# Performance work log

Hardware: AMD Instinct MI355X
Metric: run time of the kernel (lower is better)

The kernel has to match this reference:

```python
import jax, jax.numpy as jnp
import numpy as np

N = 100000
SAMPLE = 25
FEAT = 128
HIDDEN = 128
CLASSES = 40


def setup_inputs() -> dict:
    key = jax.random.key(0)
    k_x, k_n, k_w1, k_w2, k_wl = jax.random.split(key, 5)
    X = jax.random.normal(k_x, (N, FEAT), dtype=jnp.float32)
    neighbors = jax.random.randint(k_n, (N, SAMPLE), 0, N, dtype=jnp.int32)
    # torch Linear weights are [out_features, in_features], xavier-uniform init
    def xavier(k, out_d, in_d):
        bound = float(np.sqrt(6.0 / (in_d + out_d)))
        return jax.random.uniform(k, (out_d, in_d), dtype=jnp.float32, minval=-bound, maxval=bound)
    W1 = xavier(k_w1, HIDDEN, FEAT)
    W2 = xavier(k_w2, HIDDEN, HIDDEN)
    Wlast = xavier(k_wl, CLASSES, HIDDEN)
    return {"X": X, "neighbors": neighbors, "W1": W1, "W2": W2, "Wlast": Wlast}


def reference(X, neighbors, W1, W2, Wlast):
    # forward: for each layer W: X = spmm(adj, X); X = X @ W.T; relu(X)
    # adj row i has sample_num entries of value 1/sample_num -> mean over sampled neighbors
    h = X
    for W in (W1, W2):
        agg = jnp.mean(h[neighbors], axis=1)          # [N, sample, d] -> [N, d]
        h = jax.nn.relu(jnp.einsum('nd,hd->nh', agg, W))
    return jnp.einsum('nh,ch->nc', h, Wlast)          # [N, class_num]
```

## Files before the change

### kernel.cpp

```cpp
#include <hip/hip_runtime.h>
#include <cstdint>
#include <cstddef>

typedef unsigned short u16;
typedef __bf16 bf16x8 __attribute__((ext_vector_type(8)));
typedef u16 u16x8 __attribute__((ext_vector_type(8)));
typedef float f32x4 __attribute__((ext_vector_type(4)));

#define N_NODES 100000
#define SAMPLE 25
#define FEAT 128
#define CLASSES 40

__device__ __forceinline__ float bf2f(u16 v) {
    return __uint_as_float(((unsigned)v) << 16);
}
__device__ __forceinline__ u16 f2bf(float f) {
    unsigned u = __float_as_uint(f);
    u += 0x7FFFu + ((u >> 16) & 1u);
    return (u16)(u >> 16);
}
__device__ __forceinline__ void split_bf(float x, u16& hi, u16& lo) {
    hi = f2bf(x);
    lo = f2bf(x - bf2f(hi));
}

__device__ __forceinline__ void split8(const float* ap, bf16x8& ah, bf16x8& al) {
    union { u16x8 u; bf16x8 b; } H, L;
    #pragma unroll
    for (int j = 0; j < 8; ++j) {
        u16 h, lo; split_bf(ap[j], h, lo);
        H.u[j] = h; L.u[j] = lo;
    }
    ah = H.b; al = L.b;
}

__device__ __forceinline__ f32x4 mfma_split(bf16x8 ah, bf16x8 al,
                                            bf16x8 bh, bf16x8 bl, f32x4 acc) {
    acc = __builtin_amdgcn_mfma_f32_16x16x32_bf16(ah, bh, acc, 0, 0, 0);
    acc = __builtin_amdgcn_mfma_f32_16x16x32_bf16(al, bh, acc, 0, 0, 0);
    acc = __builtin_amdgcn_mfma_f32_16x16x32_bf16(ah, bl, acc, 0, 0, 0);
    return acc;
}

__device__ __forceinline__ void cex(int& a, int& b) {
    int lo = a < b ? a : b;
    int hi = a < b ? b : a;
    a = lo; b = hi;
}

__device__ __forceinline__ void sort32(int* v) {
    #pragma unroll
    for (int p = 1; p < 32; p <<= 1) {
        #pragma unroll
        for (int k = p; k >= 1; k >>= 1) {
            #pragma unroll
            for (int j = k & (p - 1); j + k < 32; j += 2 * k) {
                #pragma unroll
                for (int i = 0; i < k; ++i) {
                    if (j + i + k < 32) {
                        if (((j + i) / (2 * p)) == ((j + i + k) / (2 * p)))
                            cex(v[j + i], v[j + i + k]);
                    }
                }
            }
        }
    }
}

__global__ __launch_bounds__(256) void prep_weights(
    const float* __restrict__ W1, const float* __restrict__ W2,
    const float* __restrict__ Wl,
    u16* __restrict__ w1h, u16* __restrict__ w1l,
    u16* __restrict__ w2h, u16* __restrict__ w2l,
    u16* __restrict__ wlh, u16* __restrict__ wll)
{
    const int i = blockIdx.x * 256 + threadIdx.x;
    const int stride = gridDim.x * 256;
    for (int j = i; j < FEAT * FEAT; j += stride) {
        split_bf(W1[j], w1h[j], w1l[j]);
        split_bf(W2[j], w2h[j], w2l[j]);
    }
    for (int j = i; j < CLASSES * FEAT; j += stride) {
        split_bf(Wl[j], wlh[j], wll[j]);
    }
}

#define NPB32 32
#define ZT_STRIDE 136

__global__ __launch_bounds__(128, 4) void k1_gemm(
    const float* __restrict__ X,
    const u16* __restrict__ w1h, const u16* __restrict__ w1l,
    u16* __restrict__ Z1)
{
    __shared__ u16 zt[NPB32][ZT_STRIDE];

    const int t = threadIdx.x;
    const int w  = t >> 6;
    const int l  = t & 63;
    const int lr = l & 15;
    const int lq = l >> 4;
    const int blockStart = blockIdx.x * NPB32;
    const float* Xrow = X + (size_t)(blockStart + w * 16 + lr) * FEAT;

    bf16x8 ah[4], al[4];
    #pragma unroll
    for (int k = 0; k < 4; ++k) {
        f32x4 x0 = *(const f32x4*)(Xrow + k * 32 + lq * 8);
        f32x4 x1 = *(const f32x4*)(Xrow + k * 32 + lq * 8 + 4);
        float tmp[8];
        #pragma unroll
        for (int j = 0; j < 4; ++j) { tmp[j] = x0[j]; tmp[4 + j] = x1[j]; }
        split8(tmp, ah[k], al[k]);
    }

    #pragma unroll
    for (int c = 0; c < 8; ++c) {
        f32x4 acc = {0.f, 0.f, 0.f, 0.f};
        #pragma unroll
        for (int k = 0; k < 4; ++k) {
            const size_t off = (size_t)(c * 16 + lr) * FEAT + k * 32 + lq * 8;
            bf16x8 bh = *(const bf16x8*)(w1h + off);
            bf16x8 bl = *(const bf16x8*)(w1l + off);
            acc = mfma_split(ah[k], al[k], bh, bl, acc);
        }
        #pragma unroll
        for (int r = 0; r < 4; ++r)
            zt[w * 16 + lq * 4 + r][c * 16 + lr] = f2bf(acc[r]);
    }
    __syncthreads();

    #pragma unroll
    for (int p = 0; p < 4; ++p) {
        const int idx = p * 128 + t;
        const int row = idx >> 4;
        const int col = (idx & 15) * 8;
        *(u16x8*)(Z1 + (size_t)(blockStart + row) * FEAT + col) =
            *(const u16x8*)&zt[row][col];
    }
}

__global__ __launch_bounds__(128, 3) void k2_hop(
    const u16* __restrict__ Zin, const int* __restrict__ nb,
    const u16* __restrict__ wh, const u16* __restrict__ wl,
    u16* __restrict__ Zout)
{
    __shared__ int nbs[NPB32 * SAMPLE];
    __shared__ float agg[NPB32][132];

    const int t = threadIdx.x;
    const int blockStart = blockIdx.x * NPB32;

    for (int i = t; i < NPB32 * SAMPLE; i += 128)
        nbs[i] = nb[blockStart * SAMPLE + i];
    __syncthreads();

    if (t < NPB32) {
        int v[32];
        #pragma unroll
        for (int s = 0; s < SAMPLE; ++s) v[s] = nbs[t * SAMPLE + s];
        #pragma unroll
        for (int s = SAMPLE; s < 32; ++s) v[s] = 0x7FFFFFFF;
        sort32(v);
        #pragma unroll
        for (int s = 0; s < SAMPLE; ++s) nbs[t * SAMPLE + s] = v[s];
    }
    __syncthreads();

    #pragma unroll 1
    for (int it = 0; it < 4; ++it) {
        const int item = t + it * 128;
        const int nl = item >> 4;
        const int fg = item & 15;
        const int* myn = &nbs[nl * SAMPLE];
        u16x8 buf[SAMPLE];
        #pragma unroll
        for (int s = 0; s < SAMPLE; ++s)
            buf[s] = *(const u16x8*)(Zin + ((size_t)myn[s] << 7) + fg * 8);
        float acc[8];
        #pragma unroll
        for (int j = 0; j < 8; ++j) acc[j] = 0.f;
        #pragma unroll
        for (int s = 0; s < SAMPLE; ++s) {
            #pragma unroll
            for (int j = 0; j < 8; ++j) acc[j] += bf2f(buf[s][j]);
        }
        #pragma unroll
        for (int j = 0; j < 8; ++j) {
            float m = acc[j] * (1.0f / SAMPLE);
            agg[nl][fg * 8 + j] = m > 0.f ? m : 0.f;
        }
    }
    __syncthreads();

    const int w  = t >> 6;
    const int l  = t & 63;
    const int lr = l & 15;
    const int lq = l >> 4;

    bf16x8 ah[4], al[4];
    #pragma unroll
    for (int k = 0; k < 4; ++k)
        split8(&agg[w * 16 + lr][k * 32 + lq * 8], ah[k], al[k]);
    __syncthreads();

    u16* zt = (u16*)agg;

    #pragma unroll
    for (int c = 0; c < 8; ++c) {
        f32x4 acc = {0.f, 0.f, 0.f, 0.f};
        #pragma unroll
        for (int k = 0; k < 4; ++k) {
            const size_t off = (size_t)(c * 16 + lr) * FEAT + k * 32 + lq * 8;
            bf16x8 bh = *(const bf16x8*)(wh + off);
            bf16x8 bl = *(const bf16x8*)(wl + off);
            acc = mfma_split(ah[k], al[k], bh, bl, acc);
        }
        #pragma unroll
        for (int r = 0; r < 4; ++r)
            zt[(size_t)(w * 16 + lq * 4 + r) * ZT_STRIDE + c * 16 + lr] = f2bf(acc[r]);
    }
    __syncthreads();

    #pragma unroll
    for (int p = 0; p < 4; ++p) {
        const int idx = p * 128 + t;
        const int row = idx >> 4;
        const int col = (idx & 15) * 8;
        *(u16x8*)(Zout + (size_t)(blockStart + row) * FEAT + col) =
            *(const u16x8*)&zt[(size_t)row * ZT_STRIDE + col];
    }
}

__global__ __launch_bounds__(128, 3) void k3_hop(
    const u16* __restrict__ Zin, const int* __restrict__ nb,
    const u16* __restrict__ wh, const u16* __restrict__ wl,
    float* __restrict__ out)
{
    __shared__ int nbs[NPB32 * SAMPLE];
    __shared__ float agg[NPB32][132];

    const int t = threadIdx.x;
    const int blockStart = blockIdx.x * NPB32;

    for (int i = t; i < NPB32 * SAMPLE; i += 128)
        nbs[i] = nb[blockStart * SAMPLE + i];
    __syncthreads();

    if (t < NPB32) {
        int v[32];
        #pragma unroll
        for (int s = 0; s < SAMPLE; ++s) v[s] = nbs[t * SAMPLE + s];
        #pragma unroll
        for (int s = SAMPLE; s < 32; ++s) v[s] = 0x7FFFFFFF;
        sort32(v);
        #pragma unroll
        for (int s = 0; s < SAMPLE; ++s) nbs[t * SAMPLE + s] = v[s];
    }
    __syncthreads();

    #pragma unroll 1
    for (int it = 0; it < 4; ++it) {
        const int item = t + it * 128;
        const int nl = item >> 4;
        const int fg = item & 15;
        const int* myn = &nbs[nl * SAMPLE];
        u16x8 buf[SAMPLE];
        #pragma unroll
        for (int s = 0; s < SAMPLE; ++s)
            buf[s] = *(const u16x8*)(Zin + ((size_t)myn[s] << 7) + fg * 8);
        float acc[8];
        #pragma unroll
        for (int j = 0; j < 8; ++j) acc[j] = 0.f;
        #pragma unroll
        for (int s = 0; s < SAMPLE; ++s) {
            #pragma unroll
            for (int j = 0; j < 8; ++j) acc[j] += bf2f(buf[s][j]);
        }
        #pragma unroll
        for (int j = 0; j < 8; ++j) {
            float m = acc[j] * (1.0f / SAMPLE);
            agg[nl][fg * 8 + j] = m > 0.f ? m : 0.f;
        }
    }
    __syncthreads();

    const int w  = t >> 6;
    const int l  = t & 63;
    const int lr = l & 15;
    const int lq = l >> 4;

    bf16x8 ah[4], al[4];
    #pragma unroll
    for (int k = 0; k < 4; ++k)
        split8(&agg[w * 16 + lr][k * 32 + lq * 8], ah[k], al[k]);

    #pragma unroll
    for (int c = 0; c < 3; ++c) {
        const int o = c * 16 + lr;
        f32x4 acc = {0.f, 0.f, 0.f, 0.f};
        #pragma unroll
        for (int k = 0; k < 4; ++k) {
            bf16x8 bh, bl;
            if (o < CLASSES) {
                const size_t off = (size_t)o * FEAT + k * 32 + lq * 8;
                bh = *(const bf16x8*)(wh + off);
                bl = *(const bf16x8*)(wl + off);
            } else {
                #pragma unroll
                for (int j = 0; j < 8; ++j) { bh[j] = (__bf16)0.f; bl[j] = (__bf16)0.f; }
            }
            acc = mfma_split(ah[k], al[k], bh, bl, acc);
        }
        if (o < CLASSES) {
            #pragma unroll
            for (int r = 0; r < 4; ++r) {
                const int node = blockStart + w * 16 + lq * 4 + r;
                out[(size_t)node * CLASSES + o] = acc[r];
            }
        }
    }
}

#define NPB 64
#define AGG_STRIDE 136

__global__ __launch_bounds__(256) void gnn_layer1(
    const float* __restrict__ X, const int* __restrict__ nb,
    const u16* __restrict__ w1h, const u16* __restrict__ w1l,
    u16* __restrict__ h1)
{
    __shared__ int nbs[NPB * SAMPLE];
    __shared__ u16 agg_h[NPB][AGG_STRIDE];
    __shared__ u16 agg_l[NPB][AGG_STRIDE];

    const int t = threadIdx.x;
    const int blockStart = blockIdx.x * NPB;

    for (int i = t; i < NPB * SAMPLE; i += 256) {
        int gi = blockStart * SAMPLE + i;
        if (gi >= N_NODES * SAMPLE) gi = N_NODES * SAMPLE - 1;
        nbs[i] = nb[gi];
    }
    __syncthreads();

    for (int item = t; item < NPB * 16; item += 256) {
        const int nl = item >> 4;
        const int fg = item & 15;
        float acc[8];
        #pragma unroll
        for (int j = 0; j < 8; ++j) acc[j] = 0.f;
        const int* myn = &nbs[nl * SAMPLE];
        for (int s = 0; s < SAMPLE; ++s) {
            const float4* p = (const float4*)(X + (size_t)myn[s] * FEAT + fg * 8);
            float4 a = p[0], b = p[1];
            acc[0] += a.x; acc[1] += a.y; acc[2] += a.z; acc[3] += a.w;
            acc[4] += b.x; acc[5] += b.y; acc[6] += b.z; acc[7] += b.w;
        }
        u16x8 oh, ol;
        #pragma unroll
        for (int j = 0; j < 8; ++j) {
            float m = acc[j] * (1.0f / SAMPLE);
            u16 h, lo; split_bf(m, h, lo);
            oh[j] = h; ol[j] = lo;
        }
        *(u16x8*)&agg_h[nl][fg * 8] = oh;
        *(u16x8*)&agg_l[nl][fg * 8] = ol;
    }
    __syncthreads();

    const int w  = t >> 6;
    const int l  = t & 63;
    const int lr = l & 15;
    const int lq = l >> 4;

    bf16x8 ah[4], al[4];
    #pragma unroll
    for (int k = 0; k < 4; ++k) {
        ah[k] = *(const bf16x8*)&agg_h[w * 16 + lr][k * 32 + lq * 8];
        al[k] = *(const bf16x8*)&agg_l[w * 16 + lr][k * 32 + lq * 8];
    }

    #pragma unroll
    for (int c = 0; c < 8; ++c) {
        f32x4 acc = {0.f, 0.f, 0.f, 0.f};
        #pragma unroll
        for (int k = 0; k < 4; ++k) {
            const size_t off = (size_t)(c * 16 + lr) * FEAT + k * 32 + lq * 8;
            bf16x8 bh = *(const bf16x8*)(w1h + off);
            bf16x8 bl = *(const bf16x8*)(w1l + off);
            acc = mfma_split(ah[k], al[k], bh, bl, acc);
        }
        #pragma unroll
        for (int r = 0; r < 4; ++r) {
            int node = blockStart + w * 16 + lq * 4 + r;
            if (node < N_NODES) {
                float v = acc[r] > 0.f ? acc[r] : 0.f;
                h1[(size_t)node * FEAT + c * 16 + lr] = f2bf(v);
            }
        }
    }
}

__global__ __launch_bounds__(256) void gnn_layer2_final(
    const u16* __restrict__ h1, const int* __restrict__ nb,
    const u16* __restrict__ w2h, const u16* __restrict__ w2l,
    const u16* __restrict__ wlh, const u16* __restrict__ wll,
    float* __restrict__ out)
{
    __shared__ int nbs[NPB * SAMPLE];
    __shared__ u16 agg_h[NPB][AGG_STRIDE];
    __shared__ u16 agg_l[NPB][AGG_STRIDE];

    const int t = threadIdx.x;
    const int blockStart = blockIdx.x * NPB;

    for (int i = t; i < NPB * SAMPLE; i += 256) {
        int gi = blockStart * SAMPLE + i;
        if (gi >= N_NODES * SAMPLE) gi = N_NODES * SAMPLE - 1;
        nbs[i] = nb[gi];
    }
    __syncthreads();

    for (int item = t; item < NPB * 16; item += 256) {
        const int nl = item >> 4;
        const int fg = item & 15;
        float acc[8];
        #pragma unroll
        for (int j = 0; j < 8; ++j) acc[j] = 0.f;
        const int* myn = &nbs[nl * SAMPLE];
        for (int s = 0; s < SAMPLE; ++s) {
            u16x8 v = *(const u16x8*)(h1 + (size_t)myn[s] * FEAT + fg * 8);
            #pragma unroll
            for (int j = 0; j < 8; ++j) acc[j] += bf2f(v[j]);
        }
        u16x8 oh, ol;
        #pragma unroll
        for (int j = 0; j < 8; ++j) {
            float m = acc[j] * (1.0f / SAMPLE);
            u16 h, lo; split_bf(m, h, lo);
            oh[j] = h; ol[j] = lo;
        }
        *(u16x8*)&agg_h[nl][fg * 8] = oh;
        *(u16x8*)&agg_l[nl][fg * 8] = ol;
    }
    __syncthreads();

    const int w  = t >> 6;
    const int l  = t & 63;
    const int lr = l & 15;
    const int lq = l >> 4;

    f32x4 hacc[8];
    {
        bf16x8 ah[4], al[4];
        #pragma unroll
        for (int k = 0; k < 4; ++k) {
            ah[k] = *(const bf16x8*)&agg_h[w * 16 + lr][k * 32 + lq * 8];
            al[k] = *(const bf16x8*)&agg_l[w * 16 + lr][k * 32 + lq * 8];
        }
        #pragma unroll
        for (int c = 0; c < 8; ++c) {
            f32x4 acc = {0.f, 0.f, 0.f, 0.f};
            #pragma unroll
            for (int k = 0; k < 4; ++k) {
                const size_t off = (size_t)(c * 16 + lr) * FEAT + k * 32 + lq * 8;
                bf16x8 bh = *(const bf16x8*)(w2h + off);
                bf16x8 bl = *(const bf16x8*)(w2l + off);
                acc = mfma_split(ah[k], al[k], bh, bl, acc);
            }
            hacc[c] = acc;
        }
    }
    __syncthreads();

    #pragma unroll
    for (int c = 0; c < 8; ++c) {
        #pragma unroll
        for (int r = 0; r < 4; ++r) {
            float v = hacc[c][r] > 0.f ? hacc[c][r] : 0.f;
            u16 h, l2; split_bf(v, h, l2);
            agg_h[w * 16 + lq * 4 + r][c * 16 + lr] = h;
            agg_l[w * 16 + lq * 4 + r][c * 16 + lr] = l2;
        }
    }
    __syncthreads();

    {
        bf16x8 ah[4], al[4];
        #pragma unroll
        for (int k = 0; k < 4; ++k) {
            ah[k] = *(const bf16x8*)&agg_h[w * 16 + lr][k * 32 + lq * 8];
            al[k] = *(const bf16x8*)&agg_l[w * 16 + lr][k * 32 + lq * 8];
        }
        #pragma unroll
        for (int c = 0; c < 3; ++c) {
            const int o = c * 16 + lr;
            f32x4 acc = {0.f, 0.f, 0.f, 0.f};
            #pragma unroll
            for (int k = 0; k < 4; ++k) {
                bf16x8 bh, bl;
                if (o < CLASSES) {
                    const size_t off = (size_t)o * FEAT + k * 32 + lq * 8;
                    bh = *(const bf16x8*)(wlh + off);
                    bl = *(const bf16x8*)(wll + off);
                } else {
                    #pragma unroll
                    for (int j = 0; j < 8; ++j) { bh[j] = (__bf16)0.f; bl[j] = (__bf16)0.f; }
                }
                acc = mfma_split(ah[k], al[k], bh, bl, acc);
            }
            if (o < CLASSES) {
                #pragma unroll
                for (int r = 0; r < 4; ++r) {
                    int node = blockStart + w * 16 + lq * 4 + r;
                    if (node < N_NODES) {
                        out[(size_t)node * CLASSES + o] = acc[r];
                    }
                }
            }
        }
    }
}

extern "C" void kernel_launch(void* const* d_in, const int* in_sizes, int n_in,
                              void* d_out, int out_size, void* d_ws, size_t ws_size,
                              hipStream_t stream) {
    const float* X  = (const float*)d_in[0];
    const int*   nb = (const int*)d_in[1];
    const float* W1 = (const float*)d_in[2];
    const float* W2 = (const float*)d_in[3];
    const float* Wl = (const float*)d_in[4];
    float* out = (float*)d_out;

    const size_t zelems = (size_t)N_NODES * FEAT;
    const size_t welems = 4 * (size_t)FEAT * FEAT + 2 * (size_t)CLASSES * FEAT;
    const size_t need_fast = (2 * zelems + welems) * sizeof(u16);

    if (ws_size >= need_fast) {
        u16* Z1  = (u16*)d_ws;
        u16* Z2  = Z1 + zelems;
        u16* w1h = Z2 + zelems;
        u16* w1l = w1h + FEAT * FEAT;
        u16* w2h = w1l + FEAT * FEAT;
        u16* w2l = w2h + FEAT * FEAT;
        u16* wlh = w2l + FEAT * FEAT;
        u16* wll = wlh + CLASSES * FEAT;

        prep_weights<<<64, 256, 0, stream>>>(W1, W2, Wl, w1h, w1l, w2h, w2l, wlh, wll);
        const int blocks = N_NODES / NPB32;
        k1_gemm<<<blocks, 128, 0, stream>>>(X, w1h, w1l, Z1);
        k2_hop<<<blocks, 128, 0, stream>>>(Z1, nb, w2h, w2l, Z2);
        k3_hop<<<blocks, 128, 0, stream>>>(Z2, nb, wlh, wll, out);
    } else {
        u16* h1  = (u16*)d_ws;
        u16* w1h = h1 + zelems;
        u16* w1l = w1h + FEAT * FEAT;
        u16* w2h = w1l + FEAT * FEAT;
        u16* w2l = w2h + FEAT * FEAT;
        u16* wlh = w2l + FEAT * FEAT;
        u16* wll = wlh + CLASSES * FEAT;

        prep_weights<<<64, 256, 0, stream>>>(W1, W2, Wl, w1h, w1l, w2h, w2l, wlh, wll);
        const int blocks = (N_NODES + NPB - 1) / NPB;
        gnn_layer1<<<blocks, 256, 0, stream>>>(X, nb, w1h, w1l, h1);
        gnn_layer2_final<<<blocks, 256, 0, stream>>>(h1, nb, w2h, w2l, wlh, wll, out);
    }
}
```

Measured before the change: 330.1 us.

## Process gather in address-range chunks across two node groups per block

The hop kernels now handle two 32-node groups per block and walk the sorted neighbor lists in 16 row-range chunks. Every block tends to touch the same region of the feature table at the same time, so L2 reuse should improve. The price is a serialized per-item while loop, where the old code issued 25 loads up front; this lowers memory-level parallelism. It also holds 64 float accumulators per thread, which adds register pressure, and the grid is halved.

```diff
diff --git a/kernel.cpp b/kernel.cpp
--- a/kernel.cpp
+++ b/kernel.cpp
@@ -141,95 +141,138 @@
     }
 }
 
+#define GPB 2
+#define NGROUPS 3125
+#define NCHUNK 16
+#define CHUNK 6250
+#define K23_GRID ((NGROUPS + GPB - 1) / GPB)
+
 __global__ __launch_bounds__(128, 3) void k2_hop(
     const u16* __restrict__ Zin, const int* __restrict__ nb,
     const u16* __restrict__ wh, const u16* __restrict__ wl,
     u16* __restrict__ Zout)
 {
-    __shared__ int nbs[NPB32 * SAMPLE];
-    __shared__ float agg[NPB32][132];
+    __shared__ __align__(16) char smem[NPB32 * 130 * 4];
+    int*   nbs = (int*)smem;
+    float (*agg)[130] = (float(*)[130])smem;
 
     const int t = threadIdx.x;
-    const int blockStart = blockIdx.x * NPB32;
-
-    for (int i = t; i < NPB32 * SAMPLE; i += 128)
-        nbs[i] = nb[blockStart * SAMPLE + i];
-    __syncthreads();
-
-    if (t < NPB32) {
+    const int bg0 = blockIdx.x * GPB;
+
+    for (int i = t; i < GPB * NPB32 * SAMPLE; i += 128) {
+        const int g = i / (NPB32 * SAMPLE);
+        const int r = i - g * (NPB32 * SAMPLE);
+        const int gid = bg0 + g;
+        nbs[i] = (gid < NGROUPS) ? nb[(size_t)gid * (NPB32 * SAMPLE) + r] : 0;
+    }
+    __syncthreads();
+
+    if (t < GPB * NPB32) {
+        const int g = t >> 5, nl = t & 31;
         int v[32];
         #pragma unroll
-        for (int s = 0; s < SAMPLE; ++s) v[s] = nbs[t * SAMPLE + s];
+        for (int s = 0; s < SAMPLE; ++s) v[s] = nbs[g * (NPB32 * SAMPLE) + nl * SAMPLE + s];
         #pragma unroll
         for (int s = SAMPLE; s < 32; ++s) v[s] = 0x7FFFFFFF;
         sort32(v);
         #pragma unroll
-        for (int s = 0; s < SAMPLE; ++s) nbs[t * SAMPLE + s] = v[s];
-    }
-    __syncthreads();
+        for (int s = 0; s < SAMPLE; ++s) nbs[g * (NPB32 * SAMPLE) + nl * SAMPLE + s] = v[s];
+    }
+    __syncthreads();
+
+    float acc[GPB][4][8];
+    int   ptr[GPB][4];
+    #pragma unroll
+    for (int g = 0; g < GPB; ++g)
+        #pragma unroll
+        for (int it = 0; it < 4; ++it) {
+            ptr[g][it] = 0;
+            #pragma unroll
+            for (int j = 0; j < 8; ++j) acc[g][it][j] = 0.f;
+        }
 
     #pragma unroll 1
-    for (int it = 0; it < 4; ++it) {
-        const int item = t + it * 128;
-        const int nl = item >> 4;
-        const int fg = item & 15;
-        const int* myn = &nbs[nl * SAMPLE];
-        u16x8 buf[SAMPLE];
-        #pragma unroll
-        for (int s = 0; s < SAMPLE; ++s)
-            buf[s] = *(const u16x8*)(Zin + ((size_t)myn[s] << 7) + fg * 8);
-        float acc[8];
-        #pragma unroll
-        for (int j = 0; j < 8; ++j) acc[j] = 0.f;
-        #pragma unroll
-        for (int s = 0; s < SAMPLE; ++s) {
-            #pragma unroll
-            for (int j = 0; j < 8; ++j) acc[j] += bf2f(buf[s][j]);
-        }
-        #pragma unroll
-        for (int j = 0; j < 8; ++j) {
-            float m = acc[j] * (1.0f / SAMPLE);
-            agg[nl][fg * 8 + j] = m > 0.f ? m : 0.f;
-        }
-    }
-    __syncthreads();
+    for (int c = 0; c < NCHUNK; ++c) {
+        const int hi = (c + 1) * CHUNK;
+        #pragma unroll
+        for (int g = 0; g < GPB; ++g) {
+            #pragma unroll
+            for (int it = 0; it < 4; ++it) {
+                const int item = t + it * 128;
+                const int nl = item >> 4;
+                const int fg = item & 15;
+                const int* myn = &nbs[g * (NPB32 * SAMPLE) + nl * SAMPLE];
+                int p = ptr[g][it];
+                while (p < SAMPLE) {
+                    const int nbrow = myn[p];
+                    if (nbrow >= hi) break;
+                    u16x8 v = *(const u16x8*)(Zin + ((size_t)nbrow << 7) + fg * 8);
+                    #pragma unroll
+                    for (int j = 0; j < 8; ++j) acc[g][it][j] += bf2f(v[j]);
+                    ++p;
+                }
+                ptr[g][it] = p;
+            }
+        }
+    }
 
     const int w  = t >> 6;
     const int l  = t & 63;
     const int lr = l & 15;
     const int lq = l >> 4;
 
-    bf16x8 ah[4], al[4];
-    #pragma unroll
-    for (int k = 0; k < 4; ++k)
-        split8(&agg[w * 16 + lr][k * 32 + lq * 8], ah[k], al[k]);
-    __syncthreads();
-
-    u16* zt = (u16*)agg;
-
-    #pragma unroll
-    for (int c = 0; c < 8; ++c) {
-        f32x4 acc = {0.f, 0.f, 0.f, 0.f};
-        #pragma unroll
-        for (int k = 0; k < 4; ++k) {
-            const size_t off = (size_t)(c * 16 + lr) * FEAT + k * 32 + lq * 8;
-            bf16x8 bh = *(const bf16x8*)(wh + off);
-            bf16x8 bl = *(const bf16x8*)(wl + off);
-            acc = mfma_split(ah[k], al[k], bh, bl, acc);
-        }
-        #pragma unroll
-        for (int r = 0; r < 4; ++r)
-            zt[(size_t)(w * 16 + lq * 4 + r) * ZT_STRIDE + c * 16 + lr] = f2bf(acc[r]);
-    }
-    __syncthreads();
-
-    #pragma unroll
-    for (int p = 0; p < 4; ++p) {
-        const int idx = p * 128 + t;
-        const int row = idx >> 4;
-        const int col = (idx & 15) * 8;
-        *(u16x8*)(Zout + (size_t)(blockStart + row) * FEAT + col) =
-            *(const u16x8*)&zt[(size_t)row * ZT_STRIDE + col];
+    #pragma unroll 1
+    for (int g = 0; g < GPB; ++g) {
+        const int gid = bg0 + g;
+        if (gid >= NGROUPS) break;
+        __syncthreads();
+
+        #pragma unroll
+        for (int it = 0; it < 4; ++it) {
+            const int item = t + it * 128;
+            const int nl = item >> 4;
+            const int fg = item & 15;
+            #pragma unroll
+            for (int j = 0; j < 8; ++j) {
+                float m = acc[g][it][j] * (1.0f / SAMPLE);
+                agg[nl][fg * 8 + j] = m > 0.f ? m : 0.f;
+            }
+        }
+        __syncthreads();
+
+        bf16x8 ah[4], al[4];
+        #pragma unroll
+        for (int k = 0; k < 4; ++k)
+            split8(&agg[w * 16 + lr][k * 32 + lq * 8], ah[k], al[k]);
+        __syncthreads();
+
+        u16* zt = (u16*)smem;
+
+        #pragma unroll
+        for (int c = 0; c < 8; ++c) {
+            f32x4 o = {0.f, 0.f, 0.f, 0.f};
+            #pragma unroll
+            for (int k = 0; k < 4; ++k) {
+                const size_t off = (size_t)(c * 16 + lr) * FEAT + k * 32 + lq * 8;
+                bf16x8 bh = *(const bf16x8*)(wh + off);
+                bf16x8 bl = *(const bf16x8*)(wl + off);
+                o = mfma_split(ah[k], al[k], bh, bl, o);
+            }
+            #pragma unroll
+            for (int r = 0; r < 4; ++r)
+                zt[(size_t)(w * 16 + lq * 4 + r) * ZT_STRIDE + c * 16 + lr] = f2bf(o[r]);
+        }
+        __syncthreads();
+
+        const int blockStart = gid * NPB32;
+        #pragma unroll
+        for (int p = 0; p < 4; ++p) {
+            const int idx = p * 128 + t;
+            const int row = idx >> 4;
+            const int col = (idx & 15) * 8;
+            *(u16x8*)(Zout + (size_t)(blockStart + row) * FEAT + col) =
+                *(const u16x8*)&zt[(size_t)row * ZT_STRIDE + col];
+        }
     }
 }
 
@@ -238,86 +281,123 @@
     const u16* __restrict__ wh, const u16* __restrict__ wl,
     float* __restrict__ out)
 {
-    __shared__ int nbs[NPB32 * SAMPLE];
-    __shared__ float agg[NPB32][132];
+    __shared__ __align__(16) char smem[NPB32 * 130 * 4];
+    int*   nbs = (int*)smem;
+    float (*agg)[130] = (float(*)[130])smem;
 
     const int t = threadIdx.x;
-    const int blockStart = blockIdx.x * NPB32;
-
-    for (int i = t; i < NPB32 * SAMPLE; i += 128)
-        nbs[i] = nb[blockStart * SAMPLE + i];
-    __syncthreads();
-
-    if (t < NPB32) {
+    const int bg0 = blockIdx.x * GPB;
+
+    for (int i = t; i < GPB * NPB32 * SAMPLE; i += 128) {
+        const int g = i / (NPB32 * SAMPLE);
+        const int r = i - g * (NPB32 * SAMPLE);
+        const int gid = bg0 + g;
+        nbs[i] = (gid < NGROUPS) ? nb[(size_t)gid * (NPB32 * SAMPLE) + r] : 0;
+    }
+    __syncthreads();
+
+    if (t < GPB * NPB32) {
+        const int g = t >> 5, nl = t & 31;
         int v[32];
         #pragma unroll
-        for (int s = 0; s < SAMPLE; ++s) v[s] = nbs[t * SAMPLE + s];
+        for (int s = 0; s < SAMPLE; ++s) v[s] = nbs[g * (NPB32 * SAMPLE) + nl * SAMPLE + s];
         #pragma unroll
         for (int s = SAMPLE; s < 32; ++s) v[s] = 0x7FFFFFFF;
         sort32(v);
         #pragma unroll
-        for (int s = 0; s < SAMPLE; ++s) nbs[t * SAMPLE + s] = v[s];
-    }
-    __syncthreads();
+        for (int s = 0; s < SAMPLE; ++s) nbs[g * (NPB32 * SAMPLE) + nl * SAMPLE + s] = v[s];
+    }
+    __syncthreads();
+
+    float acc[GPB][4][8];
+    int   ptr[GPB][4];
+    #pragma unroll
+    for (int g = 0; g < GPB; ++g)
+        #pragma unroll
+        for (int it = 0; it < 4; ++it) {
+            ptr[g][it] = 0;
+            #pragma unroll
+            for (int j = 0; j < 8; ++j) acc[g][it][j] = 0.f;
+        }
 
     #pragma unroll 1
-    for (int it = 0; it < 4; ++it) {
-        const int item = t + it * 128;
-        const int nl = item >> 4;
-        const int fg = item & 15;
-        const int* myn = &nbs[nl * SAMPLE];
-        u16x8 buf[SAMPLE];
-        #pragma unroll
-        for (int s = 0; s < SAMPLE; ++s)
-            buf[s] = *(const u16x8*)(Zin + ((size_t)myn[s] << 7) + fg * 8);
-        float acc[8];
-        #pragma unroll
-        for (int j = 0; j < 8; ++j) acc[j] = 0.f;
-        #pragma unroll
-        for (int s = 0; s < SAMPLE; ++s) {
-            #pragma unroll
-            for (int j = 0; j < 8; ++j) acc[j] += bf2f(buf[s][j]);
-        }
-        #pragma unroll
-        for (int j = 0; j < 8; ++j) {
-            float m = acc[j] * (1.0f / SAMPLE);
-            agg[nl][fg * 8 + j] = m > 0.f ? m : 0.f;
-        }
-    }
-    __syncthreads();
+    for (int c = 0; c < NCHUNK; ++c) {
+        const int hi = (c + 1) * CHUNK;
+        #pragma unroll
+        for (int g = 0; g < GPB; ++g) {
+            #pragma unroll
+            for (int it = 0; it < 4; ++it) {
+                const int item = t + it * 128;
+                const int nl = item >> 4;
+                const int fg = item & 15;
+                const int* myn = &nbs[g * (NPB32 * SAMPLE) + nl * SAMPLE];
+                int p = ptr[g][it];
+                while (p < SAMPLE) {
+                    const int nbrow = myn[p];
+                    if (nbrow >= hi) break;
+                    u16x8 v = *(const u16x8*)(Zin + ((size_t)nbrow << 7) + fg * 8);
+                    #pragma unroll
+                    for (int j = 0; j < 8; ++j) acc[g][it][j] += bf2f(v[j]);
+                    ++p;
+                }
+                ptr[g][it] = p;
+            }
+        }
+    }
 
     const int w  = t >> 6;
     const int l  = t & 63;
     const int lr = l & 15;
     const int lq = l >> 4;
 
-    bf16x8 ah[4], al[4];
-    #pragma unroll
-    for (int k = 0; k < 4; ++k)
-        split8(&agg[w * 16 + lr][k * 32 + lq * 8], ah[k], al[k]);
-
-    #pragma unroll
-    for (int c = 0; c < 3; ++c) {
-        const int o = c * 16 + lr;
-        f32x4 acc = {0.f, 0.f, 0.f, 0.f};
-        #pragma unroll
-        for (int k = 0; k < 4; ++k) {
-            bf16x8 bh, bl;
+    #pragma unroll 1
+    for (int g = 0; g < GPB; ++g) {
+        const int gid = bg0 + g;
+        if (gid >= NGROUPS) break;
+        __syncthreads();
+
+        #pragma unroll
+        for (int it = 0; it < 4; ++it) {
+            const int item = t + it * 128;
+            const int nl = item >> 4;
+            const int fg = item & 15;
+            #pragma unroll
+            for (int j = 0; j < 8; ++j) {
+                float m = acc[g][it][j] * (1.0f / SAMPLE);
+                agg[nl][fg * 8 + j] = m > 0.f ? m : 0.f;
+            }
+        }
+        __syncthreads();
+
+        bf16x8 ah[4], al[4];
+        #pragma unroll
+        for (int k = 0; k < 4; ++k)
+            split8(&agg[w * 16 + lr][k * 32 + lq * 8], ah[k], al[k]);
+
+        const int blockStart = gid * NPB32;
+        #pragma unroll
+        for (int c = 0; c < 3; ++c) {
+            const int o = c * 16 + lr;
+            f32x4 acc2 = {0.f, 0.f, 0.f, 0.f};
+            #pragma unroll
+            for (int k = 0; k < 4; ++k) {
+                bf16x8 bh, bl;
+                if (o < CLASSES) {
+                    const size_t off = (size_t)o * FEAT + k * 32 + lq * 8;
+                    bh = *(const bf16x8*)(wh + off);
+                    bl = *(const bf16x8*)(wl + off);
+                } else {
+                    #pragma unroll
+                    for (int j = 0; j < 8; ++j) { bh[j] = (__bf16)0.f; bl[j] = (__bf16)0.f; }
+                }
+                acc2 = mfma_split(ah[k], al[k], bh, bl, acc2);
+            }
             if (o < CLASSES) {
-                const size_t off = (size_t)o * FEAT + k * 32 + lq * 8;
-                bh = *(const bf16x8*)(wh + off);
-                bl = *(const bf16x8*)(wl + off);
-            } else {
                 #pragma unroll
-                for (int j = 0; j < 8; ++j) { bh[j] = (__bf16)0.f; bl[j] = (__bf16)0.f; }
-            }
-            acc = mfma_split(ah[k], al[k], bh, bl, acc);
-        }
-        if (o < CLASSES) {
-            #pragma unroll
-            for (int r = 0; r < 4; ++r) {
-                const int node = blockStart + w * 16 + lq * 4 + r;
-                out[(size_t)node * CLASSES + o] = acc[r];
+                for (int r = 0; r < 4; ++r) {
+                    const int node = blockStart + w * 16 + lq * 4 + r;
+                    out[(size_t)node * CLASSES + o] = acc2[r];
+                }
             }
         }
     }
@@ -551,8 +631,8 @@
         prep_weights<<<64, 256, 0, stream>>>(W1, W2, Wl, w1h, w1l, w2h, w2l, wlh, wll);
         const int blocks = N_NODES / NPB32;
         k1_gemm<<<blocks, 128, 0, stream>>>(X, w1h, w1l, Z1);
-        k2_hop<<<blocks, 128, 0, stream>>>(Z1, nb, w2h, w2l, Z2);
-        k3_hop<<<blocks, 128, 0, stream>>>(Z2, nb, wlh, wll, out);
+        k2_hop<<<K23_GRID, 128, 0, stream>>>(Z1, nb, w2h, w2l, Z2);
+        k3_hop<<<K23_GRID, 128, 0, stream>>>(Z2, nb, wlh, wll, out);
     } else {
         u16* h1  = (u16*)d_ws;
         u16* w1h = h1 + zelems;
```

After: 907.2 us. +174.8%, slower.
